# Performance work log

Hardware: AMD Instinct MI355X
Metric: run time of the kernel (lower is better)

## Reference

```python
import jax, jax.numpy as jnp
import numpy as np

N_NODES = 50000


def _degree_norm(src, dst, n):
    # symmetric GCN normalization with self-loops already appended
    deg = jax.ops.segment_sum(jnp.ones(src.shape[0], jnp.float32), dst, num_segments=n)
    dinv = jnp.where(deg > 0, jax.lax.rsqrt(deg), 0.0)
    return dinv[src] * dinv[dst]  # [E_full]


def _gcn_layer(x, W, b, src, dst, norm, n):
    h = x @ W                                  # [N, out]
    msgs = h[src] * norm[:, None]              # gather + scale, [E_full, out]
    out = jax.ops.segment_sum(msgs, dst, num_segments=n)
    return out + b


def setup_inputs() -> dict:
    key = jax.random.key(0)
    k1, k2, k3, k4 = jax.random.split(key, 4)
    n, e, d_in, d_out = N_NODES, 800000, 256, 128
    x = jax.random.normal(k1, (n, d_in), jnp.float32)
    edge_index = jax.random.randint(k2, (2, e), 0, n, dtype=jnp.int64)
    W1 = jax.random.normal(k3, (d_in, 2 * d_out), jnp.float32) / np.sqrt(d_in)
    b1 = jnp.zeros((2 * d_out,), jnp.float32)
    W2 = jax.random.normal(k4, (2 * d_out, d_out), jnp.float32) / np.sqrt(2 * d_out)
    b2 = jnp.zeros((d_out,), jnp.float32)
    return {"x": x, "edge_index": edge_index, "W1": W1, "b1": b1, "W2": W2, "b2": b2}


def reference(x, edge_index, W1, b1, W2, b2):
    n = x.shape[0]
    loops = jnp.arange(n, dtype=edge_index.dtype)
    src = jnp.concatenate([edge_index[0], loops])
    dst = jnp.concatenate([edge_index[1], loops])
    norm = _degree_norm(src, dst, n)
    h = jax.nn.relu(_gcn_layer(x, W1, b1, src, dst, norm, n))
    h = jax.nn.relu(_gcn_layer(h, W2, b2, src, dst, norm, n))
    return h
```

## Files before the change

### kernel.cpp

```cpp
#include <hip/hip_runtime.h>
#include <hip/hip_bf16.h>


typedef __attribute__((ext_vector_type(8))) short bf16x8;
typedef __attribute__((ext_vector_type(8))) unsigned short u16x8;
typedef __attribute__((ext_vector_type(4))) float f32x4;

__device__ inline float bf2f(unsigned short u) {
    return __uint_as_float(((unsigned)u) << 16);
}
__device__ inline unsigned short f2bf(float f) {
    unsigned x = __float_as_uint(f);
    unsigned r = (x + 0x7fffu + ((x >> 16) & 1u)) >> 16;
    return (unsigned short)r;
}

__global__ void degree_kernel(const int* __restrict__ dst, unsigned* __restrict__ deg, int E) {
    int e = blockIdx.x * blockDim.x + threadIdx.x;
    if (e < E) atomicAdd(&deg[dst[e]], 1u);
}

__global__ void dinv_kernel(const unsigned* __restrict__ deg, float* __restrict__ dinv, int N) {
    int i = blockIdx.x * blockDim.x + threadIdx.x;
    if (i < N) dinv[i] = rsqrtf((float)(deg[i] + 1u));
}

#define NBIN 512

__global__ __launch_bounds__(256) void hist_lds_kernel(const unsigned* __restrict__ deg,
                                                       int* __restrict__ hist, int N) {
    __shared__ int lh[NBIN];
    const int t = threadIdx.x;
#pragma unroll
    for (int i = 0; i < NBIN / 256; i++) lh[t + i * 256] = 0;
    __syncthreads();
    int idx = blockIdx.x * 256 + t;
    if (idx < N) {
        int b = (int)deg[idx]; if (b > NBIN - 1) b = NBIN - 1;
        atomicAdd(&lh[NBIN - 1 - b], 1);
    }
    __syncthreads();
#pragma unroll
    for (int i = 0; i < NBIN / 256; i++) {
        int v = lh[t + i * 256];
        if (v) atomicAdd(&hist[t + i * 256], v);
    }
}

__global__ void scan_bins_kernel(const int* __restrict__ hist,
                                 int* __restrict__ binstart,
                                 int* __restrict__ bincur,
                                 int* __restrict__ edgebase,
                                 int* __restrict__ rowptr, int N, int E) {
    const int t = threadIdx.x;
    int cn = 0, ce = 0;
    for (int b = 0; b < NBIN; b += 64) {
        int i = b + t;
        int cnt = hist[i];
        int d = NBIN - 1 - i;
        int en = cnt * d;
        int xn = cnt, xe = en;
#pragma unroll
        for (int off = 1; off < 64; off <<= 1) {
            int yn = __shfl_up(xn, off, 64);
            int ye = __shfl_up(xe, off, 64);
            if (t >= off) { xn += yn; xe += ye; }
        }
        binstart[i] = cn + xn - cnt;
        bincur[i]   = cn + xn - cnt;
        edgebase[i] = ce + xe - en;
        cn += __shfl(xn, 63, 64);
        ce += __shfl(xe, 63, 64);
    }
    if (t == 0) rowptr[N] = E;
}

__global__ __launch_bounds__(256) void place_fused_kernel(
    const unsigned* __restrict__ deg,
    int* __restrict__ bincur,
    const int* __restrict__ binstart,
    const int* __restrict__ edgebase,
    int* __restrict__ perm, int* __restrict__ rankv,
    int* __restrict__ rowptr, int* __restrict__ cursor, int N) {
    __shared__ int lh[NBIN];
    __shared__ int base[NBIN];
    const int t = threadIdx.x;
#pragma unroll
    for (int i = 0; i < NBIN / 256; i++) lh[t + i * 256] = 0;
    __syncthreads();
    int idx = blockIdx.x * 256 + t;
    int bin = 0, lrank = 0;
    if (idx < N) {
        int b = (int)deg[idx]; if (b > NBIN - 1) b = NBIN - 1;
        bin = NBIN - 1 - b;
        lrank = atomicAdd(&lh[bin], 1);
    }
    __syncthreads();
#pragma unroll
    for (int i = 0; i < NBIN / 256; i++) {
        int v = lh[t + i * 256];
        if (v) base[t + i * 256] = atomicAdd(&bincur[t + i * 256], v);
    }
    __syncthreads();
    if (idx < N) {
        int pos = base[bin] + lrank;
        int d = NBIN - 1 - bin;
        int rp = edgebase[bin] + (pos - binstart[bin]) * d;
        perm[pos] = idx;
        rankv[idx] = pos;
        rowptr[pos] = rp;
        cursor[pos] = rp;
    }
}

__global__ __launch_bounds__(256) void fill_kernel(const int* __restrict__ src,
                                                   const int* __restrict__ dst,
                                                   const int* __restrict__ rank,
                                                   int* __restrict__ cursor,
                                                   unsigned short* __restrict__ col, int E) {
    int e = blockIdx.x * blockDim.x + threadIdx.x;
    if (e < E) {
        int d = dst[e];
        int pos = atomicAdd(&cursor[rank[d]], 1);
        col[pos] = (unsigned short)src[e];
    }
}

__global__ __launch_bounds__(256) void convert_x_kernel(const float* __restrict__ in,
                                                        const float* __restrict__ dinv,
                                                        unsigned short* __restrict__ out,
                                                        long n4, int ld4) {
    long i = (long)blockIdx.x * blockDim.x + threadIdx.x;
    if (i < n4) {
        float ds = dinv[i / ld4];
        float4 v = ((const float4*)in)[i];
        ushort4 o;
        o.x = f2bf(v.x * ds); o.y = f2bf(v.y * ds);
        o.z = f2bf(v.z * ds); o.w = f2bf(v.w * ds);
        ((ushort4*)out)[i] = o;
    }
}

__global__ __launch_bounds__(256) void convert_wt_kernel(const float* __restrict__ W,
                                                         unsigned short* __restrict__ WT,
                                                         int K, int Nw) {
    int id = blockIdx.x * blockDim.x + threadIdx.x;
    if (id < K * Nw) {
        int k = id / Nw;
        int n = id % Nw;
        WT[(long)n * K + k] = f2bf(W[id]);
    }
}

#define GBM 128
#define GBN 128
#define GBK 64
template <int CH>
__global__ __launch_bounds__(256) void gemm_bf16(const unsigned short* __restrict__ A,
                                                 const unsigned short* __restrict__ BT,
                                                 unsigned short* __restrict__ C,
                                                 int M, int Nc, int K) {
    __shared__ __align__(16) unsigned short As[GBM * GBK];
    __shared__ __align__(16) unsigned short Bs[GBN * GBK];
    const int t = threadIdx.x;
    const int lane = t & 63;
    const int w = t >> 6;
    const int row0 = blockIdx.x * GBM;
    const int col0 = blockIdx.y * GBN;
    const int rb = (w >> 1) * 64;
    const int cb = (w & 1) * 64;

    f32x4 acc[4][4] = {};

    for (int kb = 0; kb < K; kb += GBK) {
#pragma unroll
        for (int i = 0; i < 4; i++) {
            int p = i * 256 + t;
            int row = p >> 3;
            int slot = p & 7;
            int chunk = slot ^ (row & 7);
            int grow = row0 + row;
            if (grow >= M) grow = M - 1;
            const unsigned short* src = A + (size_t)grow * K + kb + chunk * 8;
            __builtin_amdgcn_global_load_lds(
                (const __attribute__((address_space(1))) void*)src,
                (__attribute__((address_space(3))) void*)&As[p * 8], 16, 0, 0);
        }
#pragma unroll
        for (int i = 0; i < 4; i++) {
            int p = i * 256 + t;
            int row = p >> 3;
            int slot = p & 7;
            int chunk = slot ^ (row & 7);
            const unsigned short* src = BT + (size_t)(col0 + row) * K + kb + chunk * 8;
            __builtin_amdgcn_global_load_lds(
                (const __attribute__((address_space(1))) void*)src,
                (__attribute__((address_space(3))) void*)&Bs[p * 8], 16, 0, 0);
        }
        asm volatile("s_waitcnt vmcnt(0)" ::: "memory");
        __syncthreads();

#pragma unroll
        for (int ks = 0; ks < 2; ks++) {
            int kq = ks * 4 + (lane >> 4);
            int rsel = lane & 15;
            bf16x8 af[4], bfr[4];
#pragma unroll
            for (int mt = 0; mt < 4; mt++) {
                int m = rb + mt * 16 + rsel;
                int slot = kq ^ (m & 7);
                af[mt] = *(const bf16x8*)&As[m * GBK + slot * 8];
            }
#pragma unroll
            for (int nt = 0; nt < 4; nt++) {
                int n = cb + nt * 16 + rsel;
                int slot = kq ^ (n & 7);
                bfr[nt] = *(const bf16x8*)&Bs[n * GBK + slot * 8];
            }
#pragma unroll
            for (int mt = 0; mt < 4; mt++)
#pragma unroll
                for (int nt = 0; nt < 4; nt++)
                    acc[mt][nt] = __builtin_amdgcn_mfma_f32_16x16x32_bf16(
                        af[mt], bfr[nt], acc[mt][nt], 0, 0, 0);
        }
        __syncthreads();
    }

#pragma unroll
    for (int mt = 0; mt < 4; mt++) {
#pragma unroll
        for (int nt = 0; nt < 4; nt++) {
            int gcol = col0 + cb + nt * 16 + (lane & 15);
            int c = gcol / CH;
            int fo = gcol % CH;
            int grow0 = row0 + rb + mt * 16 + 4 * (lane >> 4);
#pragma unroll
            for (int r = 0; r < 4; r++) {
                int g = grow0 + r;
                if (g < M)
                    C[((size_t)c * M + g) * CH + fo] = f2bf(acc[mt][nt][r]);
            }
        }
    }
}

template <int CH, int NCH, bool OUT_BF16>
__global__ __launch_bounds__(256) void gather_cm_kernel(
    const unsigned short* __restrict__ h_cm,
    const int* __restrict__ rowptr,
    const unsigned short* __restrict__ col,
    const int* __restrict__ perm,
    const float* __restrict__ dinv,
    const float* __restrict__ bias,
    void* __restrict__ out,
    int Nn, int F) {
    constexpr int LF = CH / 8;
    constexpr int NS = 64 / LF;
    constexpr int NPB = NS * 4;
    const int chunk = blockIdx.x % NCH;
    const int g = blockIdx.x / NCH;
    const int w = threadIdx.x >> 6;
    const int lane = threadIdx.x & 63;
    const int fl = lane & (LF - 1);
    const int ns = lane / LF;
    const int idx = g * NPB + w * NS + ns;
    const bool valid = idx < Nn;
    const int cidx = valid ? idx : Nn - 1;
    const int node = perm[cidx];

    const unsigned short* hc = h_cm + (size_t)chunk * Nn * CH;
    const int beg = rowptr[cidx];
    const int end = valid ? rowptr[cidx + 1] : beg;
    const float ddst = dinv[node];
    const int fo = fl * 8;

    float a0[8] = {}, a1[8] = {};
    int e = beg;
    for (; e + 8 <= end; e += 8) {
        int s0 = col[e],     s1 = col[e + 1], s2 = col[e + 2], s3 = col[e + 3];
        int s4 = col[e + 4], s5 = col[e + 5], s6 = col[e + 6], s7 = col[e + 7];
        u16x8 u0 = *(const u16x8*)(hc + s0 * CH + fo);
        u16x8 u1 = *(const u16x8*)(hc + s1 * CH + fo);
        u16x8 u2 = *(const u16x8*)(hc + s2 * CH + fo);
        u16x8 u3 = *(const u16x8*)(hc + s3 * CH + fo);
        u16x8 u4 = *(const u16x8*)(hc + s4 * CH + fo);
        u16x8 u5 = *(const u16x8*)(hc + s5 * CH + fo);
        u16x8 u6 = *(const u16x8*)(hc + s6 * CH + fo);
        u16x8 u7 = *(const u16x8*)(hc + s7 * CH + fo);
#pragma unroll
        for (int j = 0; j < 8; j++) {
            a0[j] += (bf2f(u0[j]) + bf2f(u1[j])) + (bf2f(u2[j]) + bf2f(u3[j]));
            a1[j] += (bf2f(u4[j]) + bf2f(u5[j])) + (bf2f(u6[j]) + bf2f(u7[j]));
        }
    }
    for (; e + 4 <= end; e += 4) {
        int s0 = col[e], s1 = col[e + 1], s2 = col[e + 2], s3 = col[e + 3];
        u16x8 u0 = *(const u16x8*)(hc + s0 * CH + fo);
        u16x8 u1 = *(const u16x8*)(hc + s1 * CH + fo);
        u16x8 u2 = *(const u16x8*)(hc + s2 * CH + fo);
        u16x8 u3 = *(const u16x8*)(hc + s3 * CH + fo);
#pragma unroll
        for (int j = 0; j < 8; j++) {
            a0[j] += (bf2f(u0[j]) + bf2f(u1[j])) + (bf2f(u2[j]) + bf2f(u3[j]));
        }
    }
    for (; e < end; e++) {
        int s = col[e];
        u16x8 u = *(const u16x8*)(hc + s * CH + fo);
#pragma unroll
        for (int j = 0; j < 8; j++) a1[j] += bf2f(u[j]);
    }

    if (valid) {
        u16x8 us = *(const u16x8*)(hc + node * CH + fo);
        const int f0g = chunk * CH + fo;
        f32x4 bv0 = *(const f32x4*)(bias + f0g);
        f32x4 bv1 = *(const f32x4*)(bias + f0g + 4);
        float v[8];
#pragma unroll
        for (int j = 0; j < 8; j++) {
            float b = (j < 4) ? bv0[j] : bv1[j - 4];
            float s = (a0[j] + a1[j]) + bf2f(us[j]);
            v[j] = fmaxf(fmaf(s, ddst, b), 0.f);
        }
        if (OUT_BF16) {
            u16x8 o;
#pragma unroll
            for (int j = 0; j < 8; j++) o[j] = f2bf(v[j] * ddst);
            *(u16x8*)((unsigned short*)out + (size_t)node * F + f0g) = o;
        } else {
            f32x4 o0, o1;
#pragma unroll
            for (int j = 0; j < 4; j++) { o0[j] = v[j]; o1[j] = v[j + 4]; }
            float* op = (float*)out + (size_t)node * F + f0g;
            *(f32x4*)op = o0;
            *(f32x4*)(op + 4) = o1;
        }
    }
}

extern "C" void kernel_launch(void* const* d_in, const int* in_sizes, int n_in,
                              void* d_out, int out_size, void* d_ws, size_t ws_size,
                              hipStream_t stream) {
    const float* x  = (const float*)d_in[0];
    const int* ei   = (const int*)d_in[1];
    const float* W1 = (const float*)d_in[2];
    const float* b1 = (const float*)d_in[3];
    const float* W2 = (const float*)d_in[4];
    const float* b2 = (const float*)d_in[5];

    const int DIN = 256;
    const int N = in_sizes[0] / DIN;
    const int E = in_sizes[1] / 2;
    const int H = in_sizes[3];
    const int DOUT = in_sizes[5];

    const int* src = ei;
    const int* dst = ei + E;

    char* ws = (char*)d_ws;
    unsigned* deg = (unsigned*)ws;                   ws += (size_t)N * 4;
    float* dinv   = (float*)ws;                      ws += (size_t)N * 4;
    int* rowptr   = (int*)ws;                        ws += (size_t)(N + 4) * 4;
    int* hist     = (int*)ws;                        ws += NBIN * 4;
    int* binstart = (int*)ws;                        ws += NBIN * 4;
    int* bincur   = (int*)ws;                        ws += NBIN * 4;
    int* edgebase = (int*)ws;                        ws += NBIN * 4;
    int* perm     = (int*)ws;                        ws += (size_t)N * 4;
    int* rankv    = (int*)ws;                        ws += (size_t)N * 4;
    int* cursor   = (int*)ws;                        ws += (size_t)N * 4;
    unsigned short* col = (unsigned short*)ws;       ws += (size_t)E * 2;
    unsigned short* xb  = (unsigned short*)ws;       ws += (size_t)N * DIN * 2;
    unsigned short* w1t = (unsigned short*)ws;       ws += (size_t)DIN * H * 2;
    unsigned short* w2t = (unsigned short*)ws;       ws += (size_t)H * DOUT * 2;
    unsigned short* h1b = (unsigned short*)ws;       ws += (size_t)N * H * 2;
    unsigned short* y1b = (unsigned short*)ws;       ws += (size_t)N * H * 2;
    unsigned short* h2b = xb;
    float* outp = (float*)d_out;

    hipMemsetAsync(deg, 0, (size_t)N * 4, stream);
    hipMemsetAsync(hist, 0, (size_t)NBIN * 4, stream);
    degree_kernel<<<(E + 255) / 256, 256, 0, stream>>>(dst, deg, E);
    dinv_kernel<<<(N + 255) / 256, 256, 0, stream>>>(deg, dinv, N);
    hist_lds_kernel<<<(N + 255) / 256, 256, 0, stream>>>(deg, hist, N);
    scan_bins_kernel<<<1, 64, 0, stream>>>(hist, binstart, bincur, edgebase, rowptr, N, E);
    place_fused_kernel<<<(N + 255) / 256, 256, 0, stream>>>(
        deg, bincur, binstart, edgebase, perm, rankv, rowptr, cursor, N);
    fill_kernel<<<(E + 255) / 256, 256, 0, stream>>>(src, dst, rankv, cursor, col, E);

    {
        long n4 = (long)N * DIN / 4;
        convert_x_kernel<<<(int)((n4 + 255) / 256), 256, 0, stream>>>(x, dinv, xb, n4, DIN / 4);
        convert_wt_kernel<<<(DIN * H + 255) / 256, 256, 0, stream>>>(W1, w1t, DIN, H);
        convert_wt_kernel<<<(H * DOUT + 255) / 256, 256, 0, stream>>>(W2, w2t, H, DOUT);
    }

    {
        dim3 grid((N + GBM - 1) / GBM, H / GBN);
        gemm_bf16<32><<<grid, 256, 0, stream>>>(xb, w1t, h1b, N, H, DIN);
    }
    {
        constexpr int NPB1 = (64 / (32 / 8)) * 4;
        gather_cm_kernel<32, 8, true><<<8 * ((N + NPB1 - 1) / NPB1), 256, 0, stream>>>(
            h1b, rowptr, col, perm, dinv, b1, y1b, N, H);
    }

    {
        dim3 grid((N + GBM - 1) / GBM, DOUT / GBN);
        gemm_bf16<32><<<grid, 256, 0, stream>>>(y1b, w2t, h2b, N, DOUT, H);
    }
    {
        constexpr int NPB2 = (64 / (32 / 8)) * 4;
        gather_cm_kernel<32, 4, false><<<4 * ((N + NPB2 - 1) / NPB2), 256, 0, stream>>>(
            h2b, rowptr, col, perm, dinv, b2, outp, N, DOUT);
    }
}
```

Baseline: 333.1 us.

## Pad CSR rows to multiples of eight with a zero sentinel node

Each CSR row is rounded up to a multiple of eight entries and the padding points to an extra all-zero row appended to each feature chunk. This lets the gather kernel use one unrolled loop with vectorized 16-byte column-index loads and no remainder loops. The column loads are also prefetched one iteration ahead. Gather blocks grow to 512 threads. The cost is extra padded gathers of the zero row, a larger column array, and a small kernel that zeroes the pad rows.

```diff
diff --git a/kernel.cpp b/kernel.cpp
--- a/kernel.cpp
+++ b/kernel.cpp
@@ -51,14 +51,15 @@
                                  int* __restrict__ binstart,
                                  int* __restrict__ bincur,
                                  int* __restrict__ edgebase,
-                                 int* __restrict__ rowptr, int N, int E) {
+                                 int* __restrict__ rowptr, int N) {
     const int t = threadIdx.x;
     int cn = 0, ce = 0;
     for (int b = 0; b < NBIN; b += 64) {
         int i = b + t;
         int cnt = hist[i];
         int d = NBIN - 1 - i;
-        int en = cnt * d;
+        int d8 = (d + 7) & ~7;
+        int en = cnt * d8;
         int xn = cnt, xe = en;
 #pragma unroll
         for (int off = 1; off < 64; off <<= 1) {
@@ -72,7 +73,7 @@
         cn += __shfl(xn, 63, 64);
         ce += __shfl(xe, 63, 64);
     }
-    if (t == 0) rowptr[N] = E;
+    if (t == 0) rowptr[N] = ce;
 }
 
 __global__ __launch_bounds__(256) void place_fused_kernel(
@@ -81,7 +82,8 @@
     const int* __restrict__ binstart,
     const int* __restrict__ edgebase,
     int* __restrict__ perm, int* __restrict__ rankv,
-    int* __restrict__ rowptr, int* __restrict__ cursor, int N) {
+    int* __restrict__ rowptr, int* __restrict__ cursor,
+    unsigned short* __restrict__ col, int N) {
     __shared__ int lh[NBIN];
     __shared__ int base[NBIN];
     const int t = threadIdx.x;
@@ -105,11 +107,13 @@
     if (idx < N) {
         int pos = base[bin] + lrank;
         int d = NBIN - 1 - bin;
-        int rp = edgebase[bin] + (pos - binstart[bin]) * d;
+        int d8 = (d + 7) & ~7;
+        int rp = edgebase[bin] + (pos - binstart[bin]) * d8;
         perm[pos] = idx;
         rankv[idx] = pos;
         rowptr[pos] = rp;
         cursor[pos] = rp;
+        for (int k = d; k < d8; k++) col[rp + k] = (unsigned short)N;
     }
 }
 
@@ -152,6 +156,19 @@
     }
 }
 
+__global__ void zero_pad_kernel(unsigned short* __restrict__ h1,
+                                unsigned short* __restrict__ h2, int Np1) {
+    int t = threadIdx.x;
+    if (t < 8 * 32) {
+        int c = t >> 5, f = t & 31;
+        h1[((size_t)c * Np1 + (Np1 - 1)) * 32 + f] = 0;
+    } else if (t < 12 * 32) {
+        int q = t - 256;
+        int c = q >> 5, f = q & 31;
+        h2[((size_t)c * Np1 + (Np1 - 1)) * 32 + f] = 0;
+    }
+}
+
 #define GBM 128
 #define GBN 128
 #define GBK 64
@@ -159,7 +176,7 @@
 __global__ __launch_bounds__(256) void gemm_bf16(const unsigned short* __restrict__ A,
                                                  const unsigned short* __restrict__ BT,
                                                  unsigned short* __restrict__ C,
-                                                 int M, int Nc, int K) {
+                                                 int M, int Nc, int K, int ldm) {
     __shared__ __align__(16) unsigned short As[GBM * GBK];
     __shared__ __align__(16) unsigned short Bs[GBN * GBK];
     const int t = threadIdx.x;
@@ -239,14 +256,14 @@
             for (int r = 0; r < 4; r++) {
                 int g = grow0 + r;
                 if (g < M)
-                    C[((size_t)c * M + g) * CH + fo] = f2bf(acc[mt][nt][r]);
+                    C[((size_t)c * ldm + g) * CH + fo] = f2bf(acc[mt][nt][r]);
             }
         }
     }
 }
 
 template <int CH, int NCH, bool OUT_BF16>
-__global__ __launch_bounds__(256) void gather_cm_kernel(
+__global__ __launch_bounds__(512) void gather_cm_kernel(
     const unsigned short* __restrict__ h_cm,
     const int* __restrict__ rowptr,
     const unsigned short* __restrict__ col,
@@ -257,7 +274,7 @@
     int Nn, int F) {
     constexpr int LF = CH / 8;
     constexpr int NS = 64 / LF;
-    constexpr int NPB = NS * 4;
+    constexpr int NPB = NS * 8;
     const int chunk = blockIdx.x % NCH;
     const int g = blockIdx.x / NCH;
     const int w = threadIdx.x >> 6;
@@ -269,17 +286,18 @@
     const int cidx = valid ? idx : Nn - 1;
     const int node = perm[cidx];
 
-    const unsigned short* hc = h_cm + (size_t)chunk * Nn * CH;
+    const unsigned short* hc = h_cm + (size_t)chunk * (Nn + 1) * CH;
     const int beg = rowptr[cidx];
-    const int end = valid ? rowptr[cidx + 1] : beg;
+    const int nit = (rowptr[cidx + 1] - beg) >> 3;
     const float ddst = dinv[node];
     const int fo = fl * 8;
 
     float a0[8] = {}, a1[8] = {};
-    int e = beg;
-    for (; e + 8 <= end; e += 8) {
-        int s0 = col[e],     s1 = col[e + 1], s2 = col[e + 2], s3 = col[e + 3];
-        int s4 = col[e + 4], s5 = col[e + 5], s6 = col[e + 6], s7 = col[e + 7];
+    const unsigned short* cp = col + beg;
+    u16x8 cv = *(const u16x8*)cp;
+    for (int it = 0; it < nit; ++it) {
+        int s0 = cv[0], s1 = cv[1], s2 = cv[2], s3 = cv[3];
+        int s4 = cv[4], s5 = cv[5], s6 = cv[6], s7 = cv[7];
         u16x8 u0 = *(const u16x8*)(hc + s0 * CH + fo);
         u16x8 u1 = *(const u16x8*)(hc + s1 * CH + fo);
         u16x8 u2 = *(const u16x8*)(hc + s2 * CH + fo);
@@ -288,28 +306,13 @@
         u16x8 u5 = *(const u16x8*)(hc + s5 * CH + fo);
         u16x8 u6 = *(const u16x8*)(hc + s6 * CH + fo);
         u16x8 u7 = *(const u16x8*)(hc + s7 * CH + fo);
+        cp += 8;
+        cv = *(const u16x8*)cp;
 #pragma unroll
         for (int j = 0; j < 8; j++) {
             a0[j] += (bf2f(u0[j]) + bf2f(u1[j])) + (bf2f(u2[j]) + bf2f(u3[j]));
             a1[j] += (bf2f(u4[j]) + bf2f(u5[j])) + (bf2f(u6[j]) + bf2f(u7[j]));
         }
-    }
-    for (; e + 4 <= end; e += 4) {
-        int s0 = col[e], s1 = col[e + 1], s2 = col[e + 2], s3 = col[e + 3];
-        u16x8 u0 = *(const u16x8*)(hc + s0 * CH + fo);
-        u16x8 u1 = *(const u16x8*)(hc + s1 * CH + fo);
-        u16x8 u2 = *(const u16x8*)(hc + s2 * CH + fo);
-        u16x8 u3 = *(const u16x8*)(hc + s3 * CH + fo);
-#pragma unroll
-        for (int j = 0; j < 8; j++) {
-            a0[j] += (bf2f(u0[j]) + bf2f(u1[j])) + (bf2f(u2[j]) + bf2f(u3[j]));
-        }
-    }
-    for (; e < end; e++) {
-        int s = col[e];
-        u16x8 u = *(const u16x8*)(hc + s * CH + fo);
-#pragma unroll
-        for (int j = 0; j < 8; j++) a1[j] += bf2f(u[j]);
     }
 
     if (valid) {
@@ -370,11 +373,11 @@
     int* perm     = (int*)ws;                        ws += (size_t)N * 4;
     int* rankv    = (int*)ws;                        ws += (size_t)N * 4;
     int* cursor   = (int*)ws;                        ws += (size_t)N * 4;
-    unsigned short* col = (unsigned short*)ws;       ws += (size_t)E * 2;
+    unsigned short* col = (unsigned short*)ws;       ws += (size_t)(E + 8 * N + 64) * 2;
     unsigned short* xb  = (unsigned short*)ws;       ws += (size_t)N * DIN * 2;
     unsigned short* w1t = (unsigned short*)ws;       ws += (size_t)DIN * H * 2;
     unsigned short* w2t = (unsigned short*)ws;       ws += (size_t)H * DOUT * 2;
-    unsigned short* h1b = (unsigned short*)ws;       ws += (size_t)N * H * 2;
+    unsigned short* h1b = (unsigned short*)ws;       ws += (size_t)(N + 1) * H * 2 + 1024;
     unsigned short* y1b = (unsigned short*)ws;       ws += (size_t)N * H * 2;
     unsigned short* h2b = xb;
     float* outp = (float*)d_out;
@@ -384,9 +387,9 @@
     degree_kernel<<<(E + 255) / 256, 256, 0, stream>>>(dst, deg, E);
     dinv_kernel<<<(N + 255) / 256, 256, 0, stream>>>(deg, dinv, N);
     hist_lds_kernel<<<(N + 255) / 256, 256, 0, stream>>>(deg, hist, N);
-    scan_bins_kernel<<<1, 64, 0, stream>>>(hist, binstart, bincur, edgebase, rowptr, N, E);
+    scan_bins_kernel<<<1, 64, 0, stream>>>(hist, binstart, bincur, edgebase, rowptr, N);
     place_fused_kernel<<<(N + 255) / 256, 256, 0, stream>>>(
-        deg, bincur, binstart, edgebase, perm, rankv, rowptr, cursor, N);
+        deg, bincur, binstart, edgebase, perm, rankv, rowptr, cursor, col, N);
     fill_kernel<<<(E + 255) / 256, 256, 0, stream>>>(src, dst, rankv, cursor, col, E);
 
     {
@@ -398,21 +401,22 @@
 
     {
         dim3 grid((N + GBM - 1) / GBM, H / GBN);
-        gemm_bf16<32><<<grid, 256, 0, stream>>>(xb, w1t, h1b, N, H, DIN);
-    }
+        gemm_bf16<32><<<grid, 256, 0, stream>>>(xb, w1t, h1b, N, H, DIN, N + 1);
+    }
+    zero_pad_kernel<<<1, 384, 0, stream>>>(h1b, h2b, N + 1);
     {
-        constexpr int NPB1 = (64 / (32 / 8)) * 4;
-        gather_cm_kernel<32, 8, true><<<8 * ((N + NPB1 - 1) / NPB1), 256, 0, stream>>>(
+        constexpr int NPB1 = (64 / (32 / 8)) * 8;
+        gather_cm_kernel<32, 8, true><<<8 * ((N + NPB1 - 1) / NPB1), 512, 0, stream>>>(
             h1b, rowptr, col, perm, dinv, b1, y1b, N, H);
     }
 
     {
         dim3 grid((N + GBM - 1) / GBM, DOUT / GBN);
-        gemm_bf16<32><<<grid, 256, 0, stream>>>(y1b, w2t, h2b, N, DOUT, H);
+        gemm_bf16<32><<<grid, 256, 0, stream>>>(y1b, w2t, h2b, N, DOUT, H, N + 1);
     }
     {
-        constexpr int NPB2 = (64 / (32 / 8)) * 4;
-        gather_cm_kernel<32, 4, false><<<4 * ((N + NPB2 - 1) / NPB2), 256, 0, stream>>>(
+        constexpr int NPB2 = (64 / (32 / 8)) * 8;
+        gather_cm_kernel<32, 4, false><<<4 * ((N + NPB2 - 1) / NPB2), 512, 0, stream>>>(
             h2b, rowptr, col, perm, dinv, b2, outp, N, DOUT);
     }
 }
```

Measured after the change: 337.7 us. Within noise of the previous version (+1.4%).
